# Kernel optimization log

Hardware: AMD Instinct MI355X
Metric: run time of the kernel (lower is better)

## Reference

```python
import jax, jax.numpy as jnp
import numpy as np

B, N, D, H = 8, 2048, 128, 4
DH = D // H
EPS_LN = 1e-5


def setup_inputs() -> dict:
    key = jax.random.key(0)
    ks = jax.random.split(key, 9)
    x = jax.random.normal(ks[0], (B, N, D), dtype=jnp.float32)
    u = jax.random.uniform(ks[1], (N, N), dtype=jnp.float32)
    adj = jnp.where(u > 0.5, u, 0.0)
    adj = adj.at[jnp.arange(N), jnp.arange(N)].set(1.0)
    W = jax.random.normal(ks[2], (D, D), dtype=jnp.float32) * (1.0 / np.sqrt(D))
    a_src = jax.random.normal(ks[3], (H, DH), dtype=jnp.float32) * 0.02
    a_dst = jax.random.normal(ks[4], (H, DH), dtype=jnp.float32) * 0.02
    Wo = jax.random.normal(ks[5], (D, D), dtype=jnp.float32) * (1.0 / np.sqrt(D))
    bo = jnp.zeros((D,), dtype=jnp.float32)
    gamma = jnp.ones((D,), dtype=jnp.float32)
    beta = jnp.zeros((D,), dtype=jnp.float32)
    return {"x": x, "adj_static": adj, "W": W, "a_src": a_src, "a_dst": a_dst,
            "Wo": Wo, "bo": bo, "gamma": gamma, "beta": beta}


def reference(x, adj_static, W, a_src, a_dst, Wo, bo, gamma, beta):
    # h: (B, H, N, DH)
    h = (x @ W.T).reshape(B, N, H, DH).transpose(0, 2, 1, 3)
    src = jnp.einsum('bhnd,hd->bhn', h, a_src)  # (B, H, N)
    dst = jnp.einsum('bhnd,hd->bhn', h, a_dst)  # (B, H, N)
    e = jax.nn.leaky_relu(src[..., :, None] + dst[..., None, :], 0.2)  # (B,H,N,N)
    logA = jnp.log(jnp.clip(adj_static, 1e-8))[None, None]
    mask = (adj_static > 0)[None, None]
    e = jnp.where(mask, e + logA, -jnp.inf)
    attn = jax.nn.softmax(e, axis=-1)  # dropout is identity in eval mode
    out = attn @ h  # (B, H, N, DH)
    out = out.transpose(0, 2, 1, 3).reshape(B, N, D)
    out = out @ Wo.T + bo
    y = x + out
    mu = jnp.mean(y, axis=-1, keepdims=True)
    var = jnp.mean(jnp.square(y - mu), axis=-1, keepdims=True)
    return (y - mu) * jax.lax.rsqrt(var + EPS_LN) * gamma + beta
```

## Files before the change

### kernel.cpp

```cpp
#include <hip/hip_runtime.h>

typedef short bf16x8 __attribute__((ext_vector_type(8)));
typedef _Float16 f16x8 __attribute__((ext_vector_type(8)));
typedef _Float16 f16x2 __attribute__((ext_vector_type(2)));
typedef float f32x4  __attribute__((ext_vector_type(4)));
typedef float f32x2  __attribute__((ext_vector_type(2)));
typedef int   i32x4  __attribute__((ext_vector_type(4)));
typedef unsigned int u32x2 __attribute__((ext_vector_type(2)));

#define DEV static __device__ __forceinline__
#define LOG2E 1.4426950408889634f

DEV float bfu_to_f(unsigned short s) { return __builtin_bit_cast(float, (unsigned int)s << 16); }
DEV unsigned short f_to_bf(float f) {
  unsigned int u = __builtin_bit_cast(unsigned int, f);
  u += 0x7fffu + ((u >> 16) & 1u);
  return (unsigned short)(u >> 16);
}
DEV unsigned int pack_bf_rne(float lo, float hi) {
  return (unsigned int)f_to_bf(lo) | ((unsigned int)f_to_bf(hi) << 16);
}
DEV unsigned int pk_f16(float a, float b) {
  auto h = __builtin_amdgcn_cvt_pkrtz(a, b);
  return __builtin_bit_cast(unsigned int, h);
}
DEV unsigned short f_to_f16(float a) {
  return __builtin_bit_cast(unsigned short, (_Float16)a);
}
DEV float nexp2(float x) {
#if __has_builtin(__builtin_amdgcn_exp2f)
  return __builtin_amdgcn_exp2f(x);
#else
  return exp2f(x);
#endif
}

DEV bool detect_f32(const void* adj) { return ((const float*)adj)[0] == 1.0f; }

template<bool F32> DEV float ldS(const void* p, size_t i) {
  if constexpr (F32) return ((const float*)p)[i];
  else               return bfu_to_f(((const unsigned short*)p)[i]);
}
template<bool F32> DEV void ld8f(const void* p, size_t i, float* o) {
  if constexpr (F32) {
    const float* f = (const float*)p + i;
    f32x4 a = *(const f32x4*)f, b = *(const f32x4*)(f + 4);
    o[0]=a[0]; o[1]=a[1]; o[2]=a[2]; o[3]=a[3];
    o[4]=b[0]; o[5]=b[1]; o[6]=b[2]; o[7]=b[3];
  } else {
    i32x4 w = *(const i32x4*)((const unsigned short*)p + i);
#pragma unroll
    for (int k = 0; k < 4; ++k) {
      unsigned int u = (unsigned int)w[k];
      o[2*k]   = __builtin_bit_cast(float, u << 16);
      o[2*k+1] = __builtin_bit_cast(float, u & 0xffff0000u);
    }
  }
}
template<bool F32> DEV bf16x8 ldfrag(const void* p, size_t i) {
  if constexpr (F32) {
    float o[8]; ld8f<true>(p, i, o);
    union { bf16x8 v; unsigned short u[8]; } r;
#pragma unroll
    for (int k = 0; k < 8; ++k) r.u[k] = f_to_bf(o[k]);
    return r.v;
  } else {
    return __builtin_bit_cast(bf16x8, *(const i32x4*)((const unsigned short*)p + i));
  }
}

__global__ __launch_bounds__(256) void k_prep(const void* __restrict__ adj,
                                              unsigned short* __restrict__ adjh) {
  const size_t i0 = ((size_t)blockIdx.x * 256 + threadIdx.x) * 8;
  float f[8];
  if (detect_f32(adj)) {
    ld8f<true>(adj, i0, f);
  } else {
    ld8f<false>(adj, i0, f);
  }
  i32x4 o;
#pragma unroll
  for (int k = 0; k < 4; ++k) o[k] = (int)pk_f16(f[2*k], f[2*k+1]);
  *(i32x4*)(adjh + i0) = o;
}

template<bool F32> DEV void k_h_body(const void* __restrict__ x, const void* __restrict__ W,
                                     unsigned short* __restrict__ hT,
                                     unsigned short (&t_s)[16][136]) {
  const int tid = threadIdx.x, lane = tid & 63, wave = tid >> 6;
  const int nt = blockIdx.x >> 3, ct = blockIdx.x & 7;
  const int m = lane & 15, q = lane >> 4;
  bf16x8 wf[4];
#pragma unroll
  for (int k = 0; k < 4; ++k)
    wf[k] = ldfrag<F32>(W, (size_t)(ct * 16 + m) * 128 + q * 8 + k * 32);
#pragma unroll
  for (int s = 0; s < 2; ++s) {
    const int nsub = wave * 2 + s;
    const size_t xr = (size_t)(nt * 128 + nsub * 16 + m) * 128 + q * 8;
    f32x4 acc = {0.f, 0.f, 0.f, 0.f};
#pragma unroll
    for (int k = 0; k < 4; ++k)
      acc = __builtin_amdgcn_mfma_f32_16x16x32_bf16(ldfrag<F32>(x, xr + k * 32), wf[k],
                                                    acc, 0, 0, 0);
    u32x2 w2; w2[0] = pack_bf_rne(acc[0], acc[1]); w2[1] = pack_bf_rne(acc[2], acc[3]);
    *(u32x2*)&t_s[m][nsub * 16 + q * 4] = w2;
  }
  __syncthreads();
  const int row = tid >> 4, c8 = tid & 15;
  const int chg = ct * 16 + row, hh = chg >> 5, dloc = chg & 31;
  const int ng = nt * 128 + c8 * 8, b = ng >> 11, nl = ng & 2047;
  i32x4 v = *(const i32x4*)&t_s[row][c8 * 8];
  float f[8];
#pragma unroll
  for (int k = 0; k < 4; ++k) {
    unsigned int u = (unsigned int)v[k];
    f[2*k]   = __builtin_bit_cast(float, u << 16);
    f[2*k+1] = __builtin_bit_cast(float, u & 0xffff0000u);
  }
  i32x4 o;
#pragma unroll
  for (int k = 0; k < 4; ++k) o[k] = (int)pk_f16(f[2*k], f[2*k+1]);
  *(i32x4*)(hT + ((size_t)((b * 4 + hh) * 32 + dloc)) * 2048 + nl) = o;
}
__global__ __launch_bounds__(256) void k_h(const void* x, const void* W,
                                           unsigned short* hT, const void* adj) {
  __shared__ __align__(16) unsigned short t_s[16][136];
  if (detect_f32(adj)) k_h_body<true>(x, W, hT, t_s); else k_h_body<false>(x, W, hT, t_s);
}

template<bool F32> DEV void k_sd_body(const unsigned short* __restrict__ hT,
                                      const void* __restrict__ a_src, const void* __restrict__ a_dst,
                                      unsigned int* __restrict__ rvh,
                                      unsigned short* __restrict__ Fh,
                                      unsigned short* __restrict__ Hh) {
  const int t = blockIdx.x * 256 + threadIdx.x;
  const int n = t & 2047, bh = t >> 11, hh = bh & 3;
  const unsigned short* col = hT + (size_t)bh * 32 * 2048 + n;
  float s = 0.f, d = 0.f;
#pragma unroll
  for (int dd = 0; dd < 32; ++dd) {
    const float v = (float)__builtin_bit_cast(_Float16, col[(size_t)dd * 2048]);
    s += v * ldS<F32>(a_src, hh * 32 + dd);
    d += v * ldS<F32>(a_dst, hh * 32 + dd);
  }
  const float R = nexp2(-0.8f * LOG2E * s);
  const float F = nexp2(LOG2E * d);
  const float H = nexp2(0.2f * LOG2E * d);
  rvh[t] = pk_f16(R, R);
  Fh[t] = f_to_f16(F);
  Hh[t] = f_to_f16(H);
}
__global__ __launch_bounds__(256) void k_sd(const unsigned short* hT, const void* a_src,
                                            const void* a_dst, unsigned int* rvh,
                                            unsigned short* Fh, unsigned short* Hh,
                                            const void* adj) {
  if (detect_f32(adj)) k_sd_body<true>(hT, a_src, a_dst, rvh, Fh, Hh);
  else                 k_sd_body<false>(hT, a_src, a_dst, rvh, Fh, Hh);
}

struct SmemAttn {
  unsigned char adj[2][32][272];
  unsigned char vt[2][32][272];
  unsigned short Fs[2][128];
  unsigned short Hs[2][128];
};

__global__ __launch_bounds__(256, 4) void k_attn(const unsigned short* __restrict__ adjh,
                                                 const unsigned short* __restrict__ hTh,
                                                 const unsigned int* __restrict__ rvh,
                                                 const unsigned short* __restrict__ Fh,
                                                 const unsigned short* __restrict__ Hh,
                                                 unsigned short* __restrict__ ao) {
  __shared__ __align__(16) SmemAttn sm;
  const int tid = threadIdx.x, lane = tid & 63, wave = tid >> 6;
  const int bh = blockIdx.x & 31, iblk = blockIdx.x >> 5;
  const int b = bh >> 2, hh = bh & 3;
  const int m = lane & 15, q = lane >> 4;
  const int i0 = iblk * 32;

  const int ar = tid >> 3, ac = (tid & 7) * 32;
  const bool fstg = tid < 32;

  const unsigned char* ap = (const unsigned char*)adjh + (size_t)(i0 + ar) * 4096 + ac;
  const unsigned char* vp = (const unsigned char*)hTh + ((size_t)bh * 32 + ar) * 4096 + ac;
  const unsigned short* fp = (tid < 16 ? Fh : Hh) + (size_t)bh * 2048 + (tid & 15) * 8;

  i32x4 a0r, a1r, v0r, v1r, frr;

  a0r = *(const i32x4*)(ap);      a1r = *(const i32x4*)(ap + 16);
  v0r = *(const i32x4*)(vp);      v1r = *(const i32x4*)(vp + 16);
  if (fstg) frr = *(const i32x4*)fp;
  *(i32x4*)&sm.adj[0][ar][ac]      = a0r;
  *(i32x4*)&sm.adj[0][ar][ac + 16] = a1r;
  *(i32x4*)&sm.vt[0][ar][ac]       = v0r;
  *(i32x4*)&sm.vt[0][ar][ac + 16]  = v1r;
  if (fstg) {
    unsigned short* d = (tid < 16) ? &sm.Fs[0][(tid & 15) * 8] : &sm.Hs[0][(tid & 15) * 8];
    *(i32x4*)d = frr;
  }
  __syncthreads();

  unsigned int riw[2];
#pragma unroll
  for (int it = 0; it < 2; ++it)
    riw[it] = rvh[bh * 2048 + i0 + it * 16 + m];

  f32x4 accA[2], accB[2], accD[2];
#pragma unroll
  for (int it = 0; it < 2; ++it) {
    accA[it] = f32x4{0.f,0.f,0.f,0.f};
    accB[it] = f32x4{0.f,0.f,0.f,0.f};
    accD[it] = f32x4{0.f,0.f,0.f,0.f};
  }
  const i32x4 onev = {0x3C003C00, 0x3C003C00, 0x3C003C00, 0x3C003C00};
  const f16x8 ONE8 = __builtin_bit_cast(f16x8, onev);

  const int jq = wave * 32 + q * 8;
  const int jb = jq * 2;

#pragma unroll 2
  for (int c = 0; c < 16; ++c) {
    const int cb = c & 1;
    if (c < 15) {
      const int o = (c + 1) * 256;
      a0r = *(const i32x4*)(ap + o);      a1r = *(const i32x4*)(ap + o + 16);
      v0r = *(const i32x4*)(vp + o);      v1r = *(const i32x4*)(vp + o + 16);
      if (fstg) frr = *(const i32x4*)(fp + (c + 1) * 128);
    }
    const f16x8 A0 = *(const f16x8*)&sm.vt[cb][m][jb];
    const f16x8 A1 = *(const f16x8*)&sm.vt[cb][16 + m][jb];
    const f16x8 F8 = *(const f16x8*)&sm.Fs[cb][jq];
    const f16x8 H8 = *(const f16x8*)&sm.Hs[cb][jq];
#pragma unroll
    for (int it = 0; it < 2; ++it) {
      const f16x8 aw = *(const f16x8*)&sm.adj[cb][it * 16 + m][jb];
      const i32x4 rb = {(int)riw[it], (int)riw[it], (int)riw[it], (int)riw[it]};
      const f16x8 R8 = __builtin_bit_cast(f16x8, rb);
      const f16x8 w8 = __builtin_elementwise_max(F8, R8 * H8);
      const f16x8 p8 = aw * w8;
      accA[it] = __builtin_amdgcn_mfma_f32_16x16x32_f16(A0,   p8, accA[it], 0, 0, 0);
      accB[it] = __builtin_amdgcn_mfma_f32_16x16x32_f16(A1,   p8, accB[it], 0, 0, 0);
      accD[it] = __builtin_amdgcn_mfma_f32_16x16x32_f16(ONE8, p8, accD[it], 0, 0, 0);
    }
    if (c < 15) {
      const int nb = cb ^ 1;
      *(i32x4*)&sm.adj[nb][ar][ac]      = a0r;
      *(i32x4*)&sm.adj[nb][ar][ac + 16] = a1r;
      *(i32x4*)&sm.vt[nb][ar][ac]       = v0r;
      *(i32x4*)&sm.vt[nb][ar][ac + 16]  = v1r;
      if (fstg) {
        unsigned short* d = (tid < 16) ? &sm.Fs[nb][(tid & 15) * 8] : &sm.Hs[nb][(tid & 15) * 8];
        *(i32x4*)d = frr;
      }
    }
    __syncthreads();
  }

  float* red = (float*)&sm;
  if (wave == 1 || wave == 3) {
    const int reg = (wave >> 1) * 1536;
#pragma unroll
    for (int it = 0; it < 2; ++it) {
      const int base = reg + (it * 64 + lane) * 12;
      *(f32x4*)&red[base]     = accA[it];
      *(f32x4*)&red[base + 4] = accB[it];
      red[base + 8] = accD[it][0];
    }
  }
  __syncthreads();
  if (wave == 0 || wave == 2) {
    const int reg = (wave >> 1) * 1536;
#pragma unroll
    for (int it = 0; it < 2; ++it) {
      const int base = reg + (it * 64 + lane) * 12;
      accA[it] += *(const f32x4*)&red[base];
      accB[it] += *(const f32x4*)&red[base + 4];
      accD[it][0] += red[base + 8];
    }
  }
  __syncthreads();
  if (wave == 2) {
#pragma unroll
    for (int it = 0; it < 2; ++it) {
      const int base = (it * 64 + lane) * 12;
      *(f32x4*)&red[base]     = accA[it];
      *(f32x4*)&red[base + 4] = accB[it];
      red[base + 8] = accD[it][0];
    }
  }
  __syncthreads();
  if (wave == 0) {
#pragma unroll
    for (int it = 0; it < 2; ++it) {
      const int base = (it * 64 + lane) * 12;
      const f32x4 a0 = accA[it] + *(const f32x4*)&red[base];
      const f32x4 a1 = accB[it] + *(const f32x4*)&red[base + 4];
      const float den = accD[it][0] + red[base + 8];
      const float inv = 1.f / fmaxf(den, 1e-20f);
      const int il = it * 16 + m;
      unsigned short* op = ao + ((size_t)(b * 2048) + i0 + il) * 128 + hh * 32 + q * 4;
      u32x2 w0, w1;
      w0[0] = pack_bf_rne(a0[0] * inv, a0[1] * inv);
      w0[1] = pack_bf_rne(a0[2] * inv, a0[3] * inv);
      w1[0] = pack_bf_rne(a1[0] * inv, a1[1] * inv);
      w1[1] = pack_bf_rne(a1[2] * inv, a1[3] * inv);
      *(u32x2*)op        = w0;
      *(u32x2*)(op + 16) = w1;
    }
  }
}

template<bool F32> DEV void k_out_body(const unsigned short* __restrict__ ao,
                                       const void* __restrict__ Wo, const void* __restrict__ bo,
                                       const void* __restrict__ x, const void* __restrict__ gamma,
                                       const void* __restrict__ beta, void* __restrict__ out,
                                       float (&y_s)[16][132]) {
  const int tid = threadIdx.x, lane = tid & 63, wave = tid >> 6;
  const int m = lane & 15, q = lane >> 4;
  const int rbase = blockIdx.x * 16;
  bf16x8 af[4];
#pragma unroll
  for (int k = 0; k < 4; ++k)
    af[k] = ldfrag<false>(ao, ((size_t)(rbase + m)) * 128 + q * 8 + k * 32);
  f32x4 acc[2] = {{0.f,0.f,0.f,0.f},{0.f,0.f,0.f,0.f}};
#pragma unroll
  for (int ct = 0; ct < 2; ++ct) {
    const size_t wrow = (size_t)(wave * 32 + ct * 16 + m) * 128 + q * 8;
#pragma unroll
    for (int k = 0; k < 4; ++k)
      acc[ct] = __builtin_amdgcn_mfma_f32_16x16x32_bf16(af[k], ldfrag<F32>(Wo, wrow + k * 32),
                                                        acc[ct], 0, 0, 0);
  }
#pragma unroll
  for (int ct = 0; ct < 2; ++ct) {
    const int c = wave * 32 + ct * 16 + m;
    const float bov = ldS<F32>(bo, c);
#pragma unroll
    for (int r = 0; r < 4; ++r) {
      const int row = q * 4 + r;
      y_s[row][c] = acc[ct][r] + bov + ldS<F32>(x, (size_t)(rbase + row) * 128 + c);
    }
  }
  __syncthreads();
  const int r = tid >> 4, c16 = tid & 15;
  float vals[8], sum = 0.f, sq = 0.f;
#pragma unroll
  for (int k = 0; k < 8; ++k) {
    const float v = y_s[r][c16 * 8 + k];
    vals[k] = v; sum += v; sq += v * v;
  }
#pragma unroll
  for (int msk = 1; msk < 16; msk <<= 1) {
    sum += __shfl_xor(sum, msk, 16);
    sq  += __shfl_xor(sq,  msk, 16);
  }
  const float mu  = sum * (1.f / 128.f);
  const float var = fmaxf(sq * (1.f / 128.f) - mu * mu, 0.f);
  const float rstd = rsqrtf(var + 1e-5f);
  float o[8];
#pragma unroll
  for (int k = 0; k < 8; ++k) {
    const int c = c16 * 8 + k;
    o[k] = (vals[k] - mu) * rstd * ldS<F32>(gamma, c) + ldS<F32>(beta, c);
  }
  const size_t obase = (size_t)(rbase + r) * 128 + c16 * 8;
  if constexpr (F32) {
    float* op = (float*)out + obase;
    f32x4 w0 = {o[0],o[1],o[2],o[3]}, w1 = {o[4],o[5],o[6],o[7]};
    *(f32x4*)op = w0; *(f32x4*)(op + 4) = w1;
  } else {
    union { unsigned short u[8]; i32x4 v; } ob;
#pragma unroll
    for (int k = 0; k < 8; ++k) ob.u[k] = f_to_bf(o[k]);
    *(i32x4*)((unsigned short*)out + obase) = ob.v;
  }
}
__global__ __launch_bounds__(256) void k_out(const unsigned short* ao, const void* Wo,
                                             const void* bo, const void* x, const void* gamma,
                                             const void* beta, void* out, const void* adj) {
  __shared__ __align__(16) float y_s[16][132];
  if (detect_f32(adj)) k_out_body<true>(ao, Wo, bo, x, gamma, beta, out, y_s);
  else                 k_out_body<false>(ao, Wo, bo, x, gamma, beta, out, y_s);
}

extern "C" void kernel_launch(void* const* d_in, const int* in_sizes, int n_in,
                              void* d_out, int out_size, void* d_ws, size_t ws_size,
                              hipStream_t stream) {
  const void* x     = d_in[0];
  const void* adj   = d_in[1];
  const void* W     = d_in[2];
  const void* a_src = d_in[3];
  const void* a_dst = d_in[4];
  const void* Wo    = d_in[5];
  const void* bo    = d_in[6];
  const void* gamma = d_in[7];
  const void* beta  = d_in[8];

  char* ws = (char*)d_ws;
  unsigned short* hTh   = (unsigned short*)ws;
  unsigned short* ao_ws = (unsigned short*)(ws + 4194304);
  unsigned int*   rvh   = (unsigned int*)(ws + 8388608);
  unsigned short* Fh    = (unsigned short*)(ws + 8650752);
  unsigned short* Hh    = (unsigned short*)(ws + 8781824);
  unsigned short* adjh  = (unsigned short*)(ws + 8912896);

  k_prep<<<2048, 256, 0, stream>>>(adj, adjh);
  k_h   <<<1024, 256, 0, stream>>>(x, W, hTh, adj);
  k_sd  <<<256,  256, 0, stream>>>(hTh, a_src, a_dst, rvh, Fh, Hh, adj);
  k_attn<<<2048, 256, 0, stream>>>(adjh, hTh, rvh, Fh, Hh, ao_ws);
  k_out <<<1024, 256, 0, stream>>>(ao_ws, Wo, bo, x, gamma, beta, d_out, adj);
}
```

Baseline: 148.8 us.

## Pre-swizzle adjacency and values into MFMA fragment layout, drop LDS staging in attention

The prep and projection kernels now write the f16 adjacency and transposed head values in a tiled layout that matches the MFMA operand fragment order per lane. The attention kernel then loads its operands straight from global memory with contiguous 16-byte loads per lane, removing the double-buffered shared-memory staging and the per-chunk barriers. The cost is that reuse across waves now depends on cache hits instead of LDS. Global load latency is also exposed, with no explicit prefetch beyond what the fully unrolled loop allows.

```diff
diff --git a/kernel.cpp b/kernel.cpp
--- a/kernel.cpp
+++ b/kernel.cpp
@@ -2,7 +2,6 @@
 
 typedef short bf16x8 __attribute__((ext_vector_type(8)));
 typedef _Float16 f16x8 __attribute__((ext_vector_type(8)));
-typedef _Float16 f16x2 __attribute__((ext_vector_type(2)));
 typedef float f32x4  __attribute__((ext_vector_type(4)));
 typedef float f32x2  __attribute__((ext_vector_type(2)));
 typedef int   i32x4  __attribute__((ext_vector_type(4)));
@@ -24,9 +23,7 @@
   auto h = __builtin_amdgcn_cvt_pkrtz(a, b);
   return __builtin_bit_cast(unsigned int, h);
 }
-DEV unsigned short f_to_f16(float a) {
-  return __builtin_bit_cast(unsigned short, (_Float16)a);
-}
+DEV unsigned short f_to_f16(float a) { return __builtin_bit_cast(unsigned short, (_Float16)a); }
 DEV float nexp2(float x) {
 #if __has_builtin(__builtin_amdgcn_exp2f)
   return __builtin_amdgcn_exp2f(x);
@@ -69,23 +66,25 @@
   }
 }
 
+
 __global__ __launch_bounds__(256) void k_prep(const void* __restrict__ adj,
-                                              unsigned short* __restrict__ adjh) {
-  const size_t i0 = ((size_t)blockIdx.x * 256 + threadIdx.x) * 8;
+                                              unsigned short* __restrict__ adjS) {
+  const int tid = threadIdx.x, lane = tid & 63, w = tid >> 6;
+  const int T = blockIdx.x * 4 + w;
+  const int it = T >> 6, jt = T & 63;
+  const int m = lane & 15, q = lane >> 4;
+  const size_t src = (size_t)(it * 16 + m) * 2048 + jt * 32 + q * 8;
   float f[8];
-  if (detect_f32(adj)) {
-    ld8f<true>(adj, i0, f);
-  } else {
-    ld8f<false>(adj, i0, f);
-  }
+  if (detect_f32(adj)) ld8f<true>(adj, src, f);
+  else                 ld8f<false>(adj, src, f);
   i32x4 o;
 #pragma unroll
   for (int k = 0; k < 4; ++k) o[k] = (int)pk_f16(f[2*k], f[2*k+1]);
-  *(i32x4*)(adjh + i0) = o;
+  *(i32x4*)(adjS + (size_t)T * 512 + lane * 8) = o;
 }
 
 template<bool F32> DEV void k_h_body(const void* __restrict__ x, const void* __restrict__ W,
-                                     unsigned short* __restrict__ hT,
+                                     unsigned short* __restrict__ vtS,
                                      unsigned short (&t_s)[16][136]) {
   const int tid = threadIdx.x, lane = tid & 63, wave = tid >> 6;
   const int nt = blockIdx.x >> 3, ct = blockIdx.x & 7;
@@ -121,26 +120,31 @@
   i32x4 o;
 #pragma unroll
   for (int k = 0; k < 4; ++k) o[k] = (int)pk_f16(f[2*k], f[2*k+1]);
-  *(i32x4*)(hT + ((size_t)((b * 4 + hh) * 32 + dloc)) * 2048 + nl) = o;
+  const int bh_ = b * 4 + hh;
+  const size_t idx = ((size_t)(bh_ * 2 + (dloc >> 4)) * 64 + (nl >> 5)) * 512
+                   + (((nl >> 3) & 3) * 16 + (dloc & 15)) * 8;
+  *(i32x4*)(vtS + idx) = o;
 }
 __global__ __launch_bounds__(256) void k_h(const void* x, const void* W,
-                                           unsigned short* hT, const void* adj) {
+                                           unsigned short* vtS, const void* adj) {
   __shared__ __align__(16) unsigned short t_s[16][136];
-  if (detect_f32(adj)) k_h_body<true>(x, W, hT, t_s); else k_h_body<false>(x, W, hT, t_s);
-}
-
-template<bool F32> DEV void k_sd_body(const unsigned short* __restrict__ hT,
+  if (detect_f32(adj)) k_h_body<true>(x, W, vtS, t_s); else k_h_body<false>(x, W, vtS, t_s);
+}
+
+template<bool F32> DEV void k_sd_body(const unsigned short* __restrict__ vtS,
                                       const void* __restrict__ a_src, const void* __restrict__ a_dst,
                                       unsigned int* __restrict__ rvh,
                                       unsigned short* __restrict__ Fh,
                                       unsigned short* __restrict__ Hh) {
   const int t = blockIdx.x * 256 + threadIdx.x;
   const int n = t & 2047, bh = t >> 11, hh = bh & 3;
-  const unsigned short* col = hT + (size_t)bh * 32 * 2048 + n;
+  const unsigned short* colp = vtS + ((size_t)(bh * 2) * 64 + (n >> 5)) * 512
+                             + ((n >> 3) & 3) * 128 + (n & 7);
   float s = 0.f, d = 0.f;
 #pragma unroll
   for (int dd = 0; dd < 32; ++dd) {
-    const float v = (float)__builtin_bit_cast(_Float16, col[(size_t)dd * 2048]);
+    const float v = (float)__builtin_bit_cast(_Float16,
+                      colp[(dd >> 4) * 32768 + (dd & 15) * 8]);
     s += v * ldS<F32>(a_src, hh * 32 + dd);
     d += v * ldS<F32>(a_dst, hh * 32 + dd);
   }
@@ -151,60 +155,43 @@
   Fh[t] = f_to_f16(F);
   Hh[t] = f_to_f16(H);
 }
-__global__ __launch_bounds__(256) void k_sd(const unsigned short* hT, const void* a_src,
+__global__ __launch_bounds__(256) void k_sd(const unsigned short* vtS, const void* a_src,
                                             const void* a_dst, unsigned int* rvh,
                                             unsigned short* Fh, unsigned short* Hh,
                                             const void* adj) {
-  if (detect_f32(adj)) k_sd_body<true>(hT, a_src, a_dst, rvh, Fh, Hh);
-  else                 k_sd_body<false>(hT, a_src, a_dst, rvh, Fh, Hh);
-}
-
-struct SmemAttn {
-  unsigned char adj[2][32][272];
-  unsigned char vt[2][32][272];
-  unsigned short Fs[2][128];
-  unsigned short Hs[2][128];
-};
-
-__global__ __launch_bounds__(256, 4) void k_attn(const unsigned short* __restrict__ adjh,
-                                                 const unsigned short* __restrict__ hTh,
+  if (detect_f32(adj)) k_sd_body<true>(vtS, a_src, a_dst, rvh, Fh, Hh);
+  else                 k_sd_body<false>(vtS, a_src, a_dst, rvh, Fh, Hh);
+}
+
+__global__ __launch_bounds__(256, 4) void k_attn(const unsigned short* __restrict__ adjS,
+                                                 const unsigned short* __restrict__ vtS,
                                                  const unsigned int* __restrict__ rvh,
                                                  const unsigned short* __restrict__ Fh,
                                                  const unsigned short* __restrict__ Hh,
                                                  unsigned short* __restrict__ ao) {
-  __shared__ __align__(16) SmemAttn sm;
+  __shared__ __align__(16) float red[3072];
   const int tid = threadIdx.x, lane = tid & 63, wave = tid >> 6;
   const int bh = blockIdx.x & 31, iblk = blockIdx.x >> 5;
   const int b = bh >> 2, hh = bh & 3;
   const int m = lane & 15, q = lane >> 4;
   const int i0 = iblk * 32;
-
-  const int ar = tid >> 3, ac = (tid & 7) * 32;
-  const bool fstg = tid < 32;
-
-  const unsigned char* ap = (const unsigned char*)adjh + (size_t)(i0 + ar) * 4096 + ac;
-  const unsigned char* vp = (const unsigned char*)hTh + ((size_t)bh * 32 + ar) * 4096 + ac;
-  const unsigned short* fp = (tid < 16 ? Fh : Hh) + (size_t)bh * 2048 + (tid & 15) * 8;
-
-  i32x4 a0r, a1r, v0r, v1r, frr;
-
-  a0r = *(const i32x4*)(ap);      a1r = *(const i32x4*)(ap + 16);
-  v0r = *(const i32x4*)(vp);      v1r = *(const i32x4*)(vp + 16);
-  if (fstg) frr = *(const i32x4*)fp;
-  *(i32x4*)&sm.adj[0][ar][ac]      = a0r;
-  *(i32x4*)&sm.adj[0][ar][ac + 16] = a1r;
-  *(i32x4*)&sm.vt[0][ar][ac]       = v0r;
-  *(i32x4*)&sm.vt[0][ar][ac + 16]  = v1r;
-  if (fstg) {
-    unsigned short* d = (tid < 16) ? &sm.Fs[0][(tid & 15) * 8] : &sm.Hs[0][(tid & 15) * 8];
-    *(i32x4*)d = frr;
-  }
-  __syncthreads();
-
-  unsigned int riw[2];
-#pragma unroll
-  for (int it = 0; it < 2; ++it)
-    riw[it] = rvh[bh * 2048 + i0 + it * 16 + m];
+  const int jq0 = wave * 16;
+
+  const unsigned short* ap0 = adjS + ((size_t)(iblk * 2    ) * 64 + jq0) * 512 + lane * 8;
+  const unsigned short* ap1 = adjS + ((size_t)(iblk * 2 + 1) * 64 + jq0) * 512 + lane * 8;
+  const unsigned short* vp0 = vtS + ((size_t)(bh * 2    ) * 64 + jq0) * 512 + lane * 8;
+  const unsigned short* vp1 = vtS + ((size_t)(bh * 2 + 1) * 64 + jq0) * 512 + lane * 8;
+  const unsigned short* fpF = Fh + (size_t)bh * 2048 + jq0 * 32 + q * 8;
+  const unsigned short* fpH = Hh + (size_t)bh * 2048 + jq0 * 32 + q * 8;
+
+  const unsigned int r0 = rvh[bh * 2048 + i0 + m];
+  const unsigned int r1 = rvh[bh * 2048 + i0 + 16 + m];
+  const i32x4 rb0 = {(int)r0, (int)r0, (int)r0, (int)r0};
+  const i32x4 rb1 = {(int)r1, (int)r1, (int)r1, (int)r1};
+  const f16x8 R80 = __builtin_bit_cast(f16x8, rb0);
+  const f16x8 R81 = __builtin_bit_cast(f16x8, rb1);
+  const i32x4 onev = {0x3C003C00, 0x3C003C00, 0x3C003C00, 0x3C003C00};
+  const f16x8 ONE8 = __builtin_bit_cast(f16x8, onev);
 
   f32x4 accA[2], accB[2], accD[2];
 #pragma unroll
@@ -213,51 +200,31 @@
     accB[it] = f32x4{0.f,0.f,0.f,0.f};
     accD[it] = f32x4{0.f,0.f,0.f,0.f};
   }
-  const i32x4 onev = {0x3C003C00, 0x3C003C00, 0x3C003C00, 0x3C003C00};
-  const f16x8 ONE8 = __builtin_bit_cast(f16x8, onev);
-
-  const int jq = wave * 32 + q * 8;
-  const int jb = jq * 2;
-
-#pragma unroll 2
-  for (int c = 0; c < 16; ++c) {
-    const int cb = c & 1;
-    if (c < 15) {
-      const int o = (c + 1) * 256;
-      a0r = *(const i32x4*)(ap + o);      a1r = *(const i32x4*)(ap + o + 16);
-      v0r = *(const i32x4*)(vp + o);      v1r = *(const i32x4*)(vp + o + 16);
-      if (fstg) frr = *(const i32x4*)(fp + (c + 1) * 128);
-    }
-    const f16x8 A0 = *(const f16x8*)&sm.vt[cb][m][jb];
-    const f16x8 A1 = *(const f16x8*)&sm.vt[cb][16 + m][jb];
-    const f16x8 F8 = *(const f16x8*)&sm.Fs[cb][jq];
-    const f16x8 H8 = *(const f16x8*)&sm.Hs[cb][jq];
-#pragma unroll
-    for (int it = 0; it < 2; ++it) {
-      const f16x8 aw = *(const f16x8*)&sm.adj[cb][it * 16 + m][jb];
-      const i32x4 rb = {(int)riw[it], (int)riw[it], (int)riw[it], (int)riw[it]};
-      const f16x8 R8 = __builtin_bit_cast(f16x8, rb);
-      const f16x8 w8 = __builtin_elementwise_max(F8, R8 * H8);
-      const f16x8 p8 = aw * w8;
-      accA[it] = __builtin_amdgcn_mfma_f32_16x16x32_f16(A0,   p8, accA[it], 0, 0, 0);
-      accB[it] = __builtin_amdgcn_mfma_f32_16x16x32_f16(A1,   p8, accB[it], 0, 0, 0);
-      accD[it] = __builtin_amdgcn_mfma_f32_16x16x32_f16(ONE8, p8, accD[it], 0, 0, 0);
-    }
-    if (c < 15) {
-      const int nb = cb ^ 1;
-      *(i32x4*)&sm.adj[nb][ar][ac]      = a0r;
-      *(i32x4*)&sm.adj[nb][ar][ac + 16] = a1r;
-      *(i32x4*)&sm.vt[nb][ar][ac]       = v0r;
-      *(i32x4*)&sm.vt[nb][ar][ac + 16]  = v1r;
-      if (fstg) {
-        unsigned short* d = (tid < 16) ? &sm.Fs[nb][(tid & 15) * 8] : &sm.Hs[nb][(tid & 15) * 8];
-        *(i32x4*)d = frr;
-      }
-    }
-    __syncthreads();
-  }
-
-  float* red = (float*)&sm;
+
+#pragma unroll
+  for (int j = 0; j < 16; ++j) {
+    const i32x4 a0 = *(const i32x4*)(ap0 + j * 512);
+    const i32x4 a1 = *(const i32x4*)(ap1 + j * 512);
+    const i32x4 v0 = *(const i32x4*)(vp0 + j * 512);
+    const i32x4 v1 = *(const i32x4*)(vp1 + j * 512);
+    const i32x4 ff = *(const i32x4*)(fpF + j * 32);
+    const i32x4 fh = *(const i32x4*)(fpH + j * 32);
+    const f16x8 F8 = __builtin_bit_cast(f16x8, ff);
+    const f16x8 H8 = __builtin_bit_cast(f16x8, fh);
+    const f16x8 A0 = __builtin_bit_cast(f16x8, v0);
+    const f16x8 A1 = __builtin_bit_cast(f16x8, v1);
+    const f16x8 w0 = __builtin_elementwise_max(F8, R80 * H8);
+    const f16x8 p0 = __builtin_bit_cast(f16x8, a0) * w0;
+    accA[0] = __builtin_amdgcn_mfma_f32_16x16x32_f16(A0,   p0, accA[0], 0, 0, 0);
+    accB[0] = __builtin_amdgcn_mfma_f32_16x16x32_f16(A1,   p0, accB[0], 0, 0, 0);
+    accD[0] = __builtin_amdgcn_mfma_f32_16x16x32_f16(ONE8, p0, accD[0], 0, 0, 0);
+    const f16x8 w1 = __builtin_elementwise_max(F8, R81 * H8);
+    const f16x8 p1 = __builtin_bit_cast(f16x8, a1) * w1;
+    accA[1] = __builtin_amdgcn_mfma_f32_16x16x32_f16(A0,   p1, accA[1], 0, 0, 0);
+    accB[1] = __builtin_amdgcn_mfma_f32_16x16x32_f16(A1,   p1, accB[1], 0, 0, 0);
+    accD[1] = __builtin_amdgcn_mfma_f32_16x16x32_f16(ONE8, p1, accD[1], 0, 0, 0);
+  }
+
   if (wave == 1 || wave == 3) {
     const int reg = (wave >> 1) * 1536;
 #pragma unroll
@@ -398,16 +365,16 @@
   const void* beta  = d_in[8];
 
   char* ws = (char*)d_ws;
-  unsigned short* hTh   = (unsigned short*)ws;
-  unsigned short* ao_ws = (unsigned short*)(ws + 4194304);
-  unsigned int*   rvh   = (unsigned int*)(ws + 8388608);
-  unsigned short* Fh    = (unsigned short*)(ws + 8650752);
-  unsigned short* Hh    = (unsigned short*)(ws + 8781824);
-  unsigned short* adjh  = (unsigned short*)(ws + 8912896);
-
-  k_prep<<<2048, 256, 0, stream>>>(adj, adjh);
-  k_h   <<<1024, 256, 0, stream>>>(x, W, hTh, adj);
-  k_sd  <<<256,  256, 0, stream>>>(hTh, a_src, a_dst, rvh, Fh, Hh, adj);
-  k_attn<<<2048, 256, 0, stream>>>(adjh, hTh, rvh, Fh, Hh, ao_ws);
+  unsigned short* adjS  = (unsigned short*)ws;
+  unsigned short* vtS   = (unsigned short*)(ws + 8388608);
+  unsigned short* ao_ws = (unsigned short*)(ws + 12582912);
+  unsigned int*   rvh   = (unsigned int*)(ws + 16777216);
+  unsigned short* Fh    = (unsigned short*)(ws + 17039360);
+  unsigned short* Hh    = (unsigned short*)(ws + 17170432);
+
+  k_prep<<<2048, 256, 0, stream>>>(adj, adjS);
+  k_h   <<<1024, 256, 0, stream>>>(x, W, vtS, adj);
+  k_sd  <<<256,  256, 0, stream>>>(vtS, a_src, a_dst, rvh, Fh, Hh, adj);
+  k_attn<<<2048, 256, 0, stream>>>(adjS, vtS, rvh, Fh, Hh, ao_ws);
   k_out <<<1024, 256, 0, stream>>>(ao_ws, Wo, bo, x, gamma, beta, d_out, adj);
 }
```

Result: faster. 145.4 us (-2.3%).
